# Optimization experiments

Hardware: AMD Instinct MI355X
Metric: run time of the kernel (lower is better)

## Reference

```python
import jax, jax.numpy as jnp
import numpy as np

N, CIN, COUT, K, S, H, W = 16, 512, 512, 3, 512, 64, 64
EPS = 1e-8


def setup_inputs() -> dict:
    key = jax.random.key(0)
    k1, k2, k3, k4 = jax.random.split(key, 4)
    return {
        "x": jax.random.normal(k1, (N, CIN, H, W), jnp.float32),
        "style": jax.random.normal(k2, (N, S), jnp.float32),
        # conv weight ~ N(0,1) as in the torch module (lr_mul=1)
        "weight": jax.random.normal(k3, (COUT, CIN, K, K), jnp.float32),
        # style modulation linear: weight ~ N(0,1), bias init 1.0
        "style_w": jax.random.normal(k4, (CIN, S), jnp.float32),
        "style_b": jnp.ones((CIN,), jnp.float32),
    }


def reference(x, style, weight, style_w, style_b):
    # equalized-lr scales (gain=1.0, lr_mul=1.0, mode=fan_in)
    lin_scale = 1.0 / jnp.sqrt(jnp.float32(S))          # fan_in of linear = style_channels
    w_scale = 1.0 / jnp.sqrt(jnp.float32(CIN * K * K))  # fan_in of weight[0] = Cin*k*k

    # style modulation: s[n, cin] (style_bias = 0.0)
    s = style @ (style_w.T * lin_scale) + style_b        # [N, Cin]

    w = weight * w_scale                                  # [Cout, Cin, K, K]

    # demodulation: rsqrt(sum_{i,kh,kw} (w[o,i]*s[n,i])^2 + eps) per (n, o)
    demod = jax.lax.rsqrt(jnp.einsum('oikl,ni->no', w * w, s * s) + EPS)  # [N, Cout]

    # fused form: conv(x * s, W) * demod  ==  grouped conv with per-sample modulated weights
    xs = x * s[:, :, None, None]
    out = jax.lax.conv_general_dilated(
        xs, w, window_strides=(1, 1), padding='SAME',
        dimension_numbers=('NCHW', 'OIHW', 'NCHW'))
    return out * demod[:, :, None, None]
```

## Files before the change

### kernel.cpp

```cpp
#include <hip/hip_runtime.h>
#include <hip/hip_bf16.h>

#define CIN   512
#define COUT  512
#define HW    4096
#define PADW  66
#define NB    16
#define KTOT  4608
#define BUFSZ 65536
#define BOFF  32768

static constexpr float LIN_SCALE = 0.044194173824159216f;
static constexpr float W_SCALE   = 0.014731391274719738f;

typedef __attribute__((ext_vector_type(8))) short bf16x8;
typedef __attribute__((ext_vector_type(4))) float f32x4;

__device__ __forceinline__ unsigned short f2us(float f) {
    __hip_bfloat16 h = __float2bfloat16(f); unsigned short u; __builtin_memcpy(&u, &h, 2); return u;
}

typedef const __attribute__((address_space(1))) unsigned int guint;
typedef __attribute__((address_space(3))) unsigned int luint;
__device__ __forceinline__ void gload_lds16(const void* g, void* l) {
    __builtin_amdgcn_global_load_lds((guint*)g, (luint*)l, 16, 0, 0);
}

__global__ void k_style(const float* __restrict__ style,
                        const float* __restrict__ style_w,
                        const float* __restrict__ style_b,
                        float* __restrict__ s) {
    int wid  = (blockIdx.x * blockDim.x + threadIdx.x) >> 6;
    int lane = threadIdx.x & 63;
    int n = wid >> 9, i = wid & 511;
    float sum = 0.f;
    for (int j = lane; j < 512; j += 64)
        sum += style[n * 512 + j] * style_w[i * 512 + j];
    for (int m = 32; m; m >>= 1) sum += __shfl_xor(sum, m, 64);
    if (lane == 0) s[n * 512 + i] = sum * LIN_SCALE + style_b[i];
}

__global__ void k_wprep(const float* __restrict__ weight,
                        float* __restrict__ wsq,
                        __hip_bfloat16* __restrict__ wt) {
    int oi = blockIdx.x * 256 + threadIdx.x;
    int o = oi >> 9, i = oi & 511;
    float sq = 0.f;
#pragma unroll
    for (int tp = 0; tp < 9; ++tp) {
        float v = weight[(size_t)oi * 9 + tp] * W_SCALE;
        sq += v * v;
        wt[(size_t)o * KTOT + tp * 512 + i] = __float2bfloat16(v);
    }
    wsq[oi] = sq;
}

__global__ void k_demod(const float* __restrict__ wsq, const float* __restrict__ s,
                        float* __restrict__ demod) {
    int wid  = (blockIdx.x * blockDim.x + threadIdx.x) >> 6;
    int lane = threadIdx.x & 63;
    int n = wid >> 9, o = wid & 511;
    float sum = 0.f;
    for (int i = lane; i < 512; i += 64) {
        float sv = s[n * 512 + i];
        sum += wsq[o * 512 + i] * sv * sv;
    }
    for (int m = 32; m; m >>= 1) sum += __shfl_xor(sum, m, 64);
    if (lane == 0) demod[n * 512 + o] = rsqrtf(sum + 1e-8f);
}

__global__ void k_xs(const float* __restrict__ x, const float* __restrict__ s,
                     __hip_bfloat16* __restrict__ xs) {
    const int n = blockIdx.y;
    const int t = threadIdx.x;
    if (blockIdx.x == 64) {
        uint4 z = make_uint4(0u, 0u, 0u, 0u);
        for (int idx = t; idx < 16640; idx += 256) {
            int bp = idx >> 6, sl = idx & 63;
            int hp, wp;
            if (bp < 66)       { hp = 0;  wp = bp; }
            else if (bp < 132) { hp = 65; wp = bp - 66; }
            else { int k2 = bp - 132; hp = 1 + (k2 >> 1); wp = (k2 & 1) ? 65 : 0; }
            *(uint4*)(xs + (((size_t)n * PADW * PADW) + hp * PADW + wp) * 512 + sl * 8) = z;
        }
        return;
    }
    const int h = blockIdx.x;
    const int PITCH = 65;
    __shared__ float lds[64 * 65];
    __shared__ float sv[512];
    sv[t] = s[n * 512 + t];
    sv[t + 256] = s[n * 512 + 256 + t];
    for (int ic = 0; ic < 8; ++ic) {
        const int i0 = ic * 64;
        __syncthreads();
#pragma unroll
        for (int j = 0; j < 4; ++j) {
            int idx = j * 256 + t;
            int il = idx >> 4;
            int wq = (idx & 15) * 4;
            float4 v = *(const float4*)(x + (((size_t)n * 512 + i0 + il) * HW) + h * 64 + wq);
            float* dst = &lds[il * PITCH + wq];
            dst[0] = v.x; dst[1] = v.y; dst[2] = v.z; dst[3] = v.w;
        }
        __syncthreads();
#pragma unroll
        for (int j = 0; j < 2; ++j) {
            int idx = j * 256 + t;
            int wp = idx >> 3;
            int ib = (idx & 7) * 8;
            unsigned short tmp[8];
#pragma unroll
            for (int r = 0; r < 8; ++r) {
                float xv = lds[(ib + r) * PITCH + wp];
                tmp[r] = f2us(xv * sv[i0 + ib + r]);
            }
            uint4 o;
            o.x = (unsigned)tmp[0] | ((unsigned)tmp[1] << 16);
            o.y = (unsigned)tmp[2] | ((unsigned)tmp[3] << 16);
            o.z = (unsigned)tmp[4] | ((unsigned)tmp[5] << 16);
            o.w = (unsigned)tmp[6] | ((unsigned)tmp[7] << 16);
            *(uint4*)(xs + ((size_t)((n * PADW + h + 1) * PADW + (wp + 1))) * 512 + i0 + ib) = o;
        }
    }
}

#define BAR __builtin_amdgcn_s_barrier()
#define SB0 __builtin_amdgcn_sched_barrier(0)
#define LD_B(dst, CH) { _Pragma("unroll") for (int t_ = 0; t_ < 4; ++t_) \
    dst[t_] = *(const bf16x8*)(cb + BOFF + bRow + t_ * 2048 + (CH)); }
#define LD_A(dst, MG, CH) { _Pragma("unroll") for (int t_ = 0; t_ < 4; ++t_) \
    dst[t_] = *(const bf16x8*)(cb + aRow + ((MG) * 4 + t_) * 2048 + (CH)); }
#define MFMA_G(MG, AF, BF) { __builtin_amdgcn_s_setprio(1); \
    _Pragma("unroll") for (int m_ = 0; m_ < 4; ++m_) \
    _Pragma("unroll") for (int n_ = 0; n_ < 4; ++n_) \
        acc[(MG) * 4 + m_][n_] = __builtin_amdgcn_mfma_f32_16x16x32_bf16( \
            AF[m_], BF[n_], acc[(MG) * 4 + m_][n_], 0, 0, 0); \
    __builtin_amdgcn_s_setprio(0); }

__global__ __launch_bounds__(512, 2) void k_conv(
        const __hip_bfloat16* __restrict__ wt,
        const __hip_bfloat16* __restrict__ xs,
        const float* __restrict__ demod,
        float* __restrict__ out) {
    __shared__ __attribute__((aligned(16))) char smem[2 * BUFSZ];
    const int tid  = threadIdx.x;
    const int wv   = tid >> 6, lane = tid & 63;
    const int wm   = wv >> 2,  wn   = wv & 3;

    const int bid = blockIdx.x;
    const int xcd = bid & 7, idx = bid >> 3;
    const int pT  = idx & 15;
    const int o0  = ((idx >> 4) & 1) * 256;
    const int smp = xcd * 2 + (idx >> 5);

    const __hip_bfloat16* xsn = xs + (size_t)smp * (PADW * PADW * 512);

    const int rw = lane >> 3, cl = lane & 7;
    const int lc = cl ^ rw;
    const size_t aOff = (size_t)(wv * 8 + rw) * KTOT + lc * 8;
    const size_t bOff = (size_t)(wv * 8 + rw) * 512  + lc * 8;
    const __hip_bfloat16* aStage = wt  + (size_t)o0 * KTOT + aOff;
    const __hip_bfloat16* bStage = xsn + bOff;

    const int col = lane & 15, qd = lane >> 4;
    const int ch0 = ((qd)     ^ (col & 7)) << 4;
    const int ch1 = ((qd + 4) ^ (col & 7)) << 4;
    const int aRow = (wm * 128 + col) * 128;
    const int bRow = (wn * 64  + col) * 128;

    f32x4 acc[8][4] = {};

    {
        char* nbB = smem + BOFF + wv * 1024;
        char* nbA = smem + wv * 1024;
        const __hip_bfloat16* bS = bStage + (size_t)(pT * 4) * 33792;
        gload_lds16(bS,              nbB);
        gload_lds16(bS + 33792,      nbB + 8192);
        gload_lds16(bS + 2 * 33792,  nbB + 2 * 8192);
        gload_lds16(bS + 3 * 33792,  nbB + 3 * 8192);
        gload_lds16(aStage,              nbA);
        gload_lds16(aStage + 294912,     nbA + 8192);
        gload_lds16(aStage + 2 * 294912, nbA + 2 * 8192);
        gload_lds16(aStage + 3 * 294912, nbA + 3 * 8192);
        asm volatile("s_waitcnt vmcnt(0)" ::: "memory");
        BAR;
    }

    for (int kt = 0; kt < 71; ++kt) {
        const char* cb = smem + (kt & 1) * BUFSZ;
        char* nb = smem + ((kt + 1) & 1) * BUFSZ;
        const int kt1  = kt + 1;
        const int tap1 = kt1 >> 3, c1 = kt1 & 7;
        const int kh1  = tap1 / 3, kw1 = tap1 - kh1 * 3;
        const __hip_bfloat16* aS = aStage + (size_t)kt1 * 64;
        const __hip_bfloat16* bS = bStage +
            (size_t)((pT * 4 + kh1) * PADW + kw1) * 512 + c1 * 64;
        char* nbB = nb + BOFF + wv * 1024;
        char* nbA = nb + wv * 1024;

        bf16x8 bf0[4], bf1[4], afA[4], afB[4];

        LD_B(bf0, ch0); LD_A(afA, 0, ch0); LD_A(afB, 1, ch0);
        gload_lds16(bS,             nbB);
        gload_lds16(bS + 33792,     nbB + 8192);
        gload_lds16(bS + 2 * 33792, nbB + 2 * 8192);
        gload_lds16(bS + 3 * 33792, nbB + 3 * 8192);
        BAR;
        asm volatile("s_waitcnt lgkmcnt(4)" ::: "memory"); SB0;
        MFMA_G(0, afA, bf0);
        BAR;

        LD_B(bf1, ch1); LD_A(afA, 0, ch1);
        gload_lds16(aS,              nbA);
        gload_lds16(aS + 294912,     nbA + 8192);
        gload_lds16(aS + 2 * 294912, nbA + 2 * 8192);
        gload_lds16(aS + 3 * 294912, nbA + 3 * 8192);
        BAR;
        asm volatile("s_waitcnt lgkmcnt(8)" ::: "memory"); SB0;
        MFMA_G(1, afB, bf0);
        BAR;

        LD_A(afB, 1, ch1);
        BAR;
        asm volatile("s_waitcnt lgkmcnt(4)" ::: "memory"); SB0;
        MFMA_G(0, afA, bf1);
        BAR;

        asm volatile("s_waitcnt lgkmcnt(0)" ::: "memory"); SB0;
        MFMA_G(1, afB, bf1);
        asm volatile("s_waitcnt vmcnt(0)" ::: "memory");
        BAR;
    }

    {
        const char* cb = smem + BUFSZ;
        bf16x8 bf0[4], bf1[4], afA[4], afB[4];
        LD_B(bf0, ch0); LD_A(afA, 0, ch0); MFMA_G(0, afA, bf0);
        LD_A(afB, 1, ch0);                 MFMA_G(1, afB, bf0);
        LD_B(bf1, ch1); LD_A(afA, 0, ch1); MFMA_G(0, afA, bf1);
        LD_A(afB, 1, ch1);                 MFMA_G(1, afB, bf1);
    }

    const int hwBase = pT * 256 + wn * 64 + col;
#pragma unroll
    for (int m = 0; m < 8; ++m) {
#pragma unroll
        for (int rg = 0; rg < 4; ++rg) {
            const int o = o0 + wm * 128 + m * 16 + qd * 4 + rg;
            const float dm = demod[smp * 512 + o];
            float* orow = out + ((size_t)(smp * COUT + o)) * HW + hwBase;
#pragma unroll
            for (int nn = 0; nn < 4; ++nn)
                orow[nn * 16] = acc[m][nn][rg] * dm;
        }
    }
}

extern "C" void kernel_launch(void* const* d_in, const int* in_sizes, int n_in,
                              void* d_out, int out_size, void* d_ws, size_t ws_size,
                              hipStream_t stream) {
    const float* x       = (const float*)d_in[0];
    const float* style   = (const float*)d_in[1];
    const float* weight  = (const float*)d_in[2];
    const float* style_w = (const float*)d_in[3];
    const float* style_b = (const float*)d_in[4];
    float* out = (float*)d_out;

    char* ws = (char*)d_ws;
    float*          s_buf  = (float*)(ws + 0);
    float*          wsq    = (float*)(ws + 32768);
    float*          demod  = (float*)(ws + 1081344);
    __hip_bfloat16* wt     = (__hip_bfloat16*)(ws + 1114112);
    __hip_bfloat16* xs     = (__hip_bfloat16*)(ws + 5832704);

    k_style <<<dim3(2048),     dim3(256), 0, stream>>>(style, style_w, style_b, s_buf);
    k_wprep <<<dim3(1024),     dim3(256), 0, stream>>>(weight, wsq, wt);
    k_demod <<<dim3(2048),     dim3(256), 0, stream>>>(wsq, s_buf, demod);
    k_xs    <<<dim3(65, 16),   dim3(256), 0, stream>>>(x, s_buf, xs);
    k_conv  <<<dim3(512),      dim3(512), 0, stream>>>(wt, xs, demod, out);
}
```

Before: 512.3 us.

## Use partial vmcnt waits and prefetch next tile's B fragments across iterations

```diff
diff --git a/kernel.cpp b/kernel.cpp
--- a/kernel.cpp
+++ b/kernel.cpp
@@ -127,10 +127,10 @@
 
 #define BAR __builtin_amdgcn_s_barrier()
 #define SB0 __builtin_amdgcn_sched_barrier(0)
-#define LD_B(dst, CH) { _Pragma("unroll") for (int t_ = 0; t_ < 4; ++t_) \
-    dst[t_] = *(const bf16x8*)(cb + BOFF + bRow + t_ * 2048 + (CH)); }
-#define LD_A(dst, MG, CH) { _Pragma("unroll") for (int t_ = 0; t_ < 4; ++t_) \
-    dst[t_] = *(const bf16x8*)(cb + aRow + ((MG) * 4 + t_) * 2048 + (CH)); }
+#define LD_B_AT(BASE, dst, CH) { _Pragma("unroll") for (int t_ = 0; t_ < 4; ++t_) \
+    dst[t_] = *(const bf16x8*)((BASE) + BOFF + bRow + t_ * 2048 + (CH)); }
+#define LD_A_AT(BASE, dst, MG, CH) { _Pragma("unroll") for (int t_ = 0; t_ < 4; ++t_) \
+    dst[t_] = *(const bf16x8*)((BASE) + aRow + ((MG) * 4 + t_) * 2048 + (CH)); }
 #define MFMA_G(MG, AF, BF) { __builtin_amdgcn_s_setprio(1); \
     _Pragma("unroll") for (int m_ = 0; m_ < 4; ++m_) \
     _Pragma("unroll") for (int n_ = 0; n_ < 4; ++n_) \
@@ -170,6 +170,7 @@
     const int bRow = (wn * 64  + col) * 128;
 
     f32x4 acc[8][4] = {};
+    bf16x8 bf0[4];
 
     {
         char* nbB = smem + BOFF + wv * 1024;
@@ -180,66 +181,77 @@
         gload_lds16(bS + 2 * 33792,  nbB + 2 * 8192);
         gload_lds16(bS + 3 * 33792,  nbB + 3 * 8192);
         gload_lds16(aStage,              nbA);
+        gload_lds16(aStage + 2 * 294912, nbA + 2 * 8192);
         gload_lds16(aStage + 294912,     nbA + 8192);
-        gload_lds16(aStage + 2 * 294912, nbA + 2 * 8192);
         gload_lds16(aStage + 3 * 294912, nbA + 3 * 8192);
-        asm volatile("s_waitcnt vmcnt(0)" ::: "memory");
-        BAR;
+        asm volatile("s_waitcnt vmcnt(2)" ::: "memory");
+        BAR; SB0;
+        LD_B_AT(smem, bf0, ch0);
     }
 
     for (int kt = 0; kt < 71; ++kt) {
         const char* cb = smem + (kt & 1) * BUFSZ;
-        char* nb = smem + ((kt + 1) & 1) * BUFSZ;
+        char* nb = (char*)smem + ((kt + 1) & 1) * BUFSZ;
         const int kt1  = kt + 1;
         const int tap1 = kt1 >> 3, c1 = kt1 & 7;
-        const int kh1  = tap1 / 3, kw1 = tap1 - kh1 * 3;
+        const int kh1  = (tap1 * 11) >> 5;
+        const int kw1  = tap1 - kh1 * 3;
         const __hip_bfloat16* aS = aStage + (size_t)kt1 * 64;
         const __hip_bfloat16* bS = bStage +
             (size_t)((pT * 4 + kh1) * PADW + kw1) * 512 + c1 * 64;
         char* nbB = nb + BOFF + wv * 1024;
         char* nbA = nb + wv * 1024;
 
-        bf16x8 bf0[4], bf1[4], afA[4], afB[4];
-
-        LD_B(bf0, ch0); LD_A(afA, 0, ch0); LD_A(afB, 1, ch0);
+        bf16x8 bf1[4], afE[4], afO[4];
+
+        LD_A_AT(cb, afE, 0, ch0);
         gload_lds16(bS,             nbB);
         gload_lds16(bS + 33792,     nbB + 8192);
         gload_lds16(bS + 2 * 33792, nbB + 2 * 8192);
         gload_lds16(bS + 3 * 33792, nbB + 3 * 8192);
         BAR;
+        asm volatile("s_waitcnt lgkmcnt(0)" ::: "memory"); SB0;
+        MFMA_G(0, afE, bf0);
+        asm volatile("s_waitcnt vmcnt(4)" ::: "memory");
+        BAR; SB0;
+
+        LD_A_AT(cb, afO, 1, ch0);
+        LD_B_AT(cb, bf1, ch1);
+        LD_A_AT(cb, afE, 0, ch1);
+        gload_lds16(aS,              nbA);
+        gload_lds16(aS + 2 * 294912, nbA + 2 * 8192);
+        gload_lds16(aS + 294912,     nbA + 8192);
+        gload_lds16(aS + 3 * 294912, nbA + 3 * 8192);
+        BAR;
+        asm volatile("s_waitcnt lgkmcnt(8)" ::: "memory"); SB0;
+        MFMA_G(1, afO, bf0);
+        BAR; SB0;
+
+        LD_A_AT(cb, afO, 1, ch1);
+        BAR;
         asm volatile("s_waitcnt lgkmcnt(4)" ::: "memory"); SB0;
-        MFMA_G(0, afA, bf0);
-        BAR;
-
-        LD_B(bf1, ch1); LD_A(afA, 0, ch1);
-        gload_lds16(aS,              nbA);
-        gload_lds16(aS + 294912,     nbA + 8192);
-        gload_lds16(aS + 2 * 294912, nbA + 2 * 8192);
-        gload_lds16(aS + 3 * 294912, nbA + 3 * 8192);
-        BAR;
-        asm volatile("s_waitcnt lgkmcnt(8)" ::: "memory"); SB0;
-        MFMA_G(1, afB, bf0);
-        BAR;
-
-        LD_A(afB, 1, ch1);
+        MFMA_G(0, afE, bf1);
+        asm volatile("s_waitcnt vmcnt(4)" ::: "memory");
+        BAR; SB0;
+
+        LD_B_AT(nb, bf0, ch0);
         BAR;
         asm volatile("s_waitcnt lgkmcnt(4)" ::: "memory"); SB0;
-        MFMA_G(0, afA, bf1);
-        BAR;
-
-        asm volatile("s_waitcnt lgkmcnt(0)" ::: "memory"); SB0;
-        MFMA_G(1, afB, bf1);
-        asm volatile("s_waitcnt vmcnt(0)" ::: "memory");
-        BAR;
+        MFMA_G(1, afO, bf1);
+        asm volatile("s_waitcnt vmcnt(2)" ::: "memory");
+        BAR; SB0;
     }
 
     {
         const char* cb = smem + BUFSZ;
-        bf16x8 bf0[4], bf1[4], afA[4], afB[4];
-        LD_B(bf0, ch0); LD_A(afA, 0, ch0); MFMA_G(0, afA, bf0);
-        LD_A(afB, 1, ch0);                 MFMA_G(1, afB, bf0);
-        LD_B(bf1, ch1); LD_A(afA, 0, ch1); MFMA_G(0, afA, bf1);
-        LD_A(afB, 1, ch1);                 MFMA_G(1, afB, bf1);
+        asm volatile("s_waitcnt vmcnt(0)" ::: "memory");
+        BAR; SB0;
+        bf16x8 bf1[4], afE[4], afO[4];
+        LD_A_AT(cb, afE, 0, ch0); MFMA_G(0, afE, bf0);
+        LD_A_AT(cb, afO, 1, ch0); MFMA_G(1, afO, bf0);
+        LD_B_AT(cb, bf1, ch1);
+        LD_A_AT(cb, afE, 0, ch1); MFMA_G(0, afE, bf1);
+        LD_A_AT(cb, afO, 1, ch1); MFMA_G(1, afO, bf1);
     }
 
     const int hwBase = pT * 256 + wn * 64 + col;
```

New measurement: 508.8 us. No clear change (-0.7%).
